# Kernel optimization log

Hardware: AMD Instinct MI355X
Metric: run time of the kernel (lower is better)

Reference implementation:

```python
import jax, jax.numpy as jnp
import numpy as np

N = 100000   # nodes
E = 1600000  # edges (avg degree 16)
D = 64       # in = hidden = out channels
NEG_SLOPE = 0.2
EPS_IN = 1e-5


def setup_inputs() -> dict:
    key = jax.random.key(0)
    ks = jax.random.split(key, 24)
    s = 0.05
    p = lambda k, shape: jax.random.normal(k, shape, jnp.float32) * s
    inp = {
        "x": jax.random.normal(ks[0], (N, D), jnp.float32),
        "edge_index": jax.random.randint(ks[1], (2, E), 0, N, dtype=jnp.int64),
        "edge_attr": jax.random.normal(ks[2], (E, D), jnp.float32),
        # GATv2Conv #1: lin_l, lin_r (bias=True), lin_edge (bias=False), att, out bias
        "Wl1": p(ks[3], (D, D)), "bl1": p(ks[4], (D,)),
        "Wr1": p(ks[5], (D, D)), "br1": p(ks[6], (D,)),
        "We1": p(ks[7], (D, D)), "att1": p(ks[8], (D,)), "bo1": p(ks[9], (D,)),
        # GATv2Conv #2
        "Wl2": p(ks[10], (D, D)), "bl2": p(ks[11], (D,)),
        "Wr2": p(ks[12], (D, D)), "br2": p(ks[13], (D,)),
        "We2": p(ks[14], (D, D)), "att2": p(ks[15], (D,)), "bo2": p(ks[16], (D,)),
        # skip linear
        "Wskip": p(ks[17], (D, D)), "bskip": p(ks[18], (D,)),
    }
    return inp


def _instance_norm(h):
    # InstanceNorm1d on a 2D [N, C] input -> per-row normalization over C, no affine
    mu = h.mean(-1, keepdims=True)
    var = ((h - mu) ** 2).mean(-1, keepdims=True)
    return (h - mu) * jax.lax.rsqrt(var + EPS_IN)


def _gatv2(x, src, dst, edge_attr, Wl, bl, Wr, br, We, att, bo):
    xl = x @ Wl.T + bl          # source-side transform [N, D]
    xr = x @ Wr.T + br          # target-side transform [N, D]
    e = edge_attr @ We.T        # edge transform [E, D]
    m = xl[src] + xr[dst] + e   # per-edge pre-activation [E, D]
    score = jnp.where(m > 0, m, NEG_SLOPE * m) @ att  # [E]
    # segment softmax over edges sharing the same target node
    smax = jax.ops.segment_max(score, dst, num_segments=N)
    smax = jnp.where(jnp.isfinite(smax), smax, 0.0)
    es = jnp.exp(score - smax[dst])
    denom = jax.ops.segment_sum(es, dst, num_segments=N)
    alpha = es / (denom[dst] + 1e-16)  # [E]
    out = jax.ops.segment_sum(alpha[:, None] * xl[src], dst, num_segments=N)
    return out + bo


def reference(x, edge_index, edge_attr,
              Wl1, bl1, Wr1, br1, We1, att1, bo1,
              Wl2, bl2, Wr2, br2, We2, att2, bo2,
              Wskip, bskip):
    src, dst = edge_index[0], edge_index[1]
    h = jax.nn.relu(_gatv2(x, src, dst, edge_attr, Wl1, bl1, Wr1, br1, We1, att1, bo1))
    h = _instance_norm(h)
    h2 = jax.nn.relu(_gatv2(h, src, dst, edge_attr, Wl2, bl2, Wr2, br2, We2, att2, bo2)
                     + x @ Wskip.T + bskip)
    return _instance_norm(h2)
```

## Files before the change

### kernel.cpp

```cpp
#include <hip/hip_runtime.h>

#define DCH 64
#define NEG 0.2f

typedef float fx4 __attribute__((ext_vector_type(4)));
typedef short short8 __attribute__((ext_vector_type(8)));

__device__ __forceinline__ unsigned short f2bf(float f) {
    unsigned int u = __builtin_bit_cast(unsigned int, f);
    u += 0x7fffu + ((u >> 16) & 1u);
    return (unsigned short)(u >> 16);
}

__device__ __forceinline__ short8 pack_bf16x8(fx4 a, fx4 b) {
    short8 r;
    r[0] = (short)f2bf(a[0]); r[1] = (short)f2bf(a[1]);
    r[2] = (short)f2bf(a[2]); r[3] = (short)f2bf(a[3]);
    r[4] = (short)f2bf(b[0]); r[5] = (short)f2bf(b[1]);
    r[6] = (short)f2bf(b[2]); r[7] = (short)f2bf(b[3]);
    return r;
}

__global__ void k_zero(int* __restrict__ p, int n) {
    int i = blockIdx.x * blockDim.x + threadIdx.x;
    if (i < n) p[i] = 0;
}

__global__ void k_count(const int* __restrict__ ei, int* __restrict__ deg, int E) {
    int e = blockIdx.x * blockDim.x + threadIdx.x;
    if (e < E) atomicAdd(&deg[ei[E + e]], 1);
}

__global__ void k_scan1(const int* __restrict__ deg, int* __restrict__ rowptr,
                        int* __restrict__ bsum, int n) {
    __shared__ int s[256];
    int t = threadIdx.x;
    int base = blockIdx.x * 1024 + t * 4;
    int v[4]; int sum = 0;
    #pragma unroll
    for (int j = 0; j < 4; j++) {
        int idx = base + j;
        v[j] = (idx < n) ? deg[idx] : 0;
        sum += v[j];
    }
    s[t] = sum;
    __syncthreads();
    for (int o = 1; o < 256; o <<= 1) {
        int add = (t >= o) ? s[t - o] : 0;
        __syncthreads();
        s[t] += add;
        __syncthreads();
    }
    int excl = s[t] - sum;
    if (t == 255) bsum[blockIdx.x] = s[255];
    int run = excl;
    #pragma unroll
    for (int j = 0; j < 4; j++) {
        int idx = base + j;
        if (idx < n) rowptr[idx] = run;
        run += v[j];
    }
}

__global__ void k_scan2(int* __restrict__ bsum, int nb) {
    int run = 0;
    for (int i = 0; i < nb; i++) { int t = bsum[i]; bsum[i] = run; run += t; }
}

__global__ void k_scan3(int* __restrict__ rowptr, const int* __restrict__ bsum,
                        int n, int E) {
    int i = blockIdx.x * blockDim.x + threadIdx.x;
    if (i < n) rowptr[i] += bsum[i >> 10];
    if (i == 0) rowptr[n] = E;
}

__global__ void k_fill(const int* __restrict__ ei, const int* __restrict__ rowptr,
                       int* __restrict__ cnt, int* __restrict__ csrc,
                       int* __restrict__ ceid, int E) {
    int e = blockIdx.x * blockDim.x + threadIdx.x;
    if (e < E) {
        int t = ei[E + e];
        int p = rowptr[t] + atomicAdd(&cnt[t], 1);
        csrc[p] = ei[e];
        ceid[p] = e;
    }
}

__global__ __launch_bounds__(256) void k_node_gemm(
    const float* __restrict__ X, int nrows,
    const float* __restrict__ W0, const float* __restrict__ b0, float* __restrict__ O0,
    const float* __restrict__ W1, const float* __restrict__ b1, float* __restrict__ O1,
    const float* __restrict__ W2, const float* __restrict__ b2, float* __restrict__ O2)
{
    int wid = (blockIdx.x * blockDim.x + threadIdx.x) >> 6;
    int lane = threadIdx.x & 63;
    int ntiles = (nrows + 63) >> 6;
    if (wid >= ntiles) return;
    int base = wid * 64;
    int l15 = lane & 15, q = lane >> 4;

    short8 afr[4][2];
    #pragma unroll
    for (int mt = 0; mt < 4; mt++) {
        int row = base + mt * 16 + l15;
        if (row >= nrows) row = nrows - 1;
        const float* xp = X + (size_t)row * DCH + q * 8;
        #pragma unroll
        for (int kt = 0; kt < 2; kt++) {
            fx4 v0 = *(const fx4*)(xp + kt * 32);
            fx4 v1 = *(const fx4*)(xp + kt * 32 + 4);
            afr[mt][kt] = pack_bf16x8(v0, v1);
        }
    }

    const float* Ws[3] = {W0, W1, W2};
    const float* bs[3] = {b0, b1, b2};
    float* Os[3] = {O0, O1, O2};
    int nmat = O2 ? 3 : (O1 ? 2 : 1);

    for (int m = 0; m < nmat; m++) {
        const float* W = Ws[m];
        short8 bfr[4][2];
        #pragma unroll
        for (int nt = 0; nt < 4; nt++) {
            const float* wp = W + (nt * 16 + l15) * DCH + q * 8;
            #pragma unroll
            for (int kt = 0; kt < 2; kt++) {
                fx4 v0 = *(const fx4*)(wp + kt * 32);
                fx4 v1 = *(const fx4*)(wp + kt * 32 + 4);
                bfr[nt][kt] = pack_bf16x8(v0, v1);
            }
        }
        fx4 acc[4][4] = {};
        #pragma unroll
        for (int kt = 0; kt < 2; kt++)
            #pragma unroll
            for (int mt = 0; mt < 4; mt++)
                #pragma unroll
                for (int nt = 0; nt < 4; nt++)
                    acc[mt][nt] = __builtin_amdgcn_mfma_f32_16x16x32_bf16(
                        afr[mt][kt], bfr[nt][kt], acc[mt][nt], 0, 0, 0);

        float bias[4];
        #pragma unroll
        for (int nt = 0; nt < 4; nt++) bias[nt] = bs[m][nt * 16 + l15];
        float* O = Os[m];
        #pragma unroll
        for (int mt = 0; mt < 4; mt++) {
            #pragma unroll
            for (int r = 0; r < 4; r++) {
                int row = base + mt * 16 + q * 4 + r;
                if (row < nrows) {
                    #pragma unroll
                    for (int nt = 0; nt < 4; nt++)
                        O[(size_t)row * DCH + nt * 16 + l15] = acc[mt][nt][r] + bias[nt];
                }
            }
        }
    }
}

__global__ __launch_bounds__(256) void k_edge_score(
    const float* __restrict__ EA, const int* __restrict__ ei,
    const float* __restrict__ We, const float* __restrict__ att,
    const float* __restrict__ xl, const float* __restrict__ xr,
    float* __restrict__ es, int E)
{
    int wid = (blockIdx.x * blockDim.x + threadIdx.x) >> 6;
    int lane = threadIdx.x & 63;
    int l15 = lane & 15, q = lane >> 4;
    int base = wid * 64;
    if (base >= E) return;

    int s_me = ei[base + lane];
    int t_me = ei[E + base + lane];

    short8 bfr[4][2];
    #pragma unroll
    for (int nt = 0; nt < 4; nt++) {
        const float* wp = We + (nt * 16 + l15) * DCH + q * 8;
        #pragma unroll
        for (int kt = 0; kt < 2; kt++) {
            fx4 v0 = *(const fx4*)(wp + kt * 32);
            fx4 v1 = *(const fx4*)(wp + kt * 32 + 4);
            bfr[nt][kt] = pack_bf16x8(v0, v1);
        }
    }
    short8 afr[4][2];
    #pragma unroll
    for (int mt = 0; mt < 4; mt++) {
        const float* p = EA + (size_t)(base + mt * 16 + l15) * DCH + q * 8;
        #pragma unroll
        for (int kt = 0; kt < 2; kt++) {
            fx4 v0 = *(const fx4*)(p + kt * 32);
            fx4 v1 = *(const fx4*)(p + kt * 32 + 4);
            afr[mt][kt] = pack_bf16x8(v0, v1);
        }
    }
    fx4 acc[4][4] = {};
    #pragma unroll
    for (int kt = 0; kt < 2; kt++)
        #pragma unroll
        for (int mt = 0; mt < 4; mt++)
            #pragma unroll
            for (int nt = 0; nt < 4; nt++)
                acc[mt][nt] = __builtin_amdgcn_mfma_f32_16x16x32_bf16(
                    afr[mt][kt], bfr[nt][kt], acc[mt][nt], 0, 0, 0);

    float attr[4];
    #pragma unroll
    for (int nt = 0; nt < 4; nt++) attr[nt] = att[nt * 16 + l15];

    #pragma unroll
    for (int mt = 0; mt < 4; mt++) {
        #pragma unroll
        for (int r = 0; r < 4; r++) {
            int m = mt * 16 + q * 4 + r;
            int sm = __shfl(s_me, m);
            int tm = __shfl(t_me, m);
            const float* xls = xl + (size_t)sm * DCH + l15;
            const float* xrt = xr + (size_t)tm * DCH + l15;
            float p = 0.f;
            #pragma unroll
            for (int nt = 0; nt < 4; nt++) {
                float z = acc[mt][nt][r] + xls[nt * 16] + xrt[nt * 16];
                float lr = fmaxf(z, 0.f) + NEG * fminf(z, 0.f);
                p = fmaf(attr[nt], lr, p);
            }
            p += __shfl_xor(p, 1);
            p += __shfl_xor(p, 2);
            p += __shfl_xor(p, 4);
            p += __shfl_xor(p, 8);
            if (l15 == mt * 4 + r) es[base + m] = __expf(p);
        }
    }
}

__global__ __launch_bounds__(256) void k_pull(
    const int* __restrict__ rowptr, const int* __restrict__ csrc,
    const int* __restrict__ ceid, const float* __restrict__ es,
    const float* __restrict__ xl, const float* __restrict__ bo,
    const float* __restrict__ skip, float* __restrict__ out, int n_nodes)
{
    int wid = (blockIdx.x * blockDim.x + threadIdx.x) >> 6;
    int lane = threadIdx.x & 63;
    if (wid >= n_nodes) return;
    int r0 = rowptr[wid], r1 = rowptr[wid + 1];
    float acc = 0.f, den = 0.f;
    for (int b = r0; b < r1; b += 64) {
        int cnt = min(64, r1 - b);
        int sj = 0; float wj = 0.f;
        if (lane < cnt) {
            sj = csrc[b + lane];
            wj = es[ceid[b + lane]];
        }
        for (int i = 0; i < cnt; i++) {
            int s = __shfl(sj, i);
            float w = __shfl(wj, i);
            acc = fmaf(w, xl[(size_t)s * DCH + lane], acc);
            den += w;
        }
    }
    float v = acc / (den + 1e-16f) + bo[lane];
    if (skip) v += skip[(size_t)wid * DCH + lane];
    v = fmaxf(v, 0.f);
    float mu = v;
    #pragma unroll
    for (int o = 1; o < 64; o <<= 1) mu += __shfl_xor(mu, o);
    mu *= (1.f / 64.f);
    float d = v - mu;
    float var = d * d;
    #pragma unroll
    for (int o = 1; o < 64; o <<= 1) var += __shfl_xor(var, o);
    var *= (1.f / 64.f);
    out[(size_t)wid * DCH + lane] = d * rsqrtf(var + 1e-5f);
}

extern "C" void kernel_launch(void* const* d_in, const int* in_sizes, int n_in,
                              void* d_out, int out_size, void* d_ws, size_t ws_size,
                              hipStream_t stream) {
    const float* x    = (const float*)d_in[0];
    const int*   ei   = (const int*)d_in[1];
    const float* ea   = (const float*)d_in[2];
    const float* Wl1  = (const float*)d_in[3];
    const float* bl1  = (const float*)d_in[4];
    const float* Wr1  = (const float*)d_in[5];
    const float* br1  = (const float*)d_in[6];
    const float* We1  = (const float*)d_in[7];
    const float* att1 = (const float*)d_in[8];
    const float* bo1  = (const float*)d_in[9];
    const float* Wl2  = (const float*)d_in[10];
    const float* bl2  = (const float*)d_in[11];
    const float* Wr2  = (const float*)d_in[12];
    const float* br2  = (const float*)d_in[13];
    const float* We2  = (const float*)d_in[14];
    const float* att2 = (const float*)d_in[15];
    const float* bo2  = (const float*)d_in[16];
    const float* Wsk  = (const float*)d_in[17];
    const float* bsk  = (const float*)d_in[18];
    float* out = (float*)d_out;

    const int N = in_sizes[0] / DCH;
    const int E = in_sizes[1] / 2;

    char* ws = (char*)d_ws;
    size_t off = 0;
    float* xl   = (float*)(ws + off); off += (size_t)N * DCH * 4;
    float* xr   = (float*)(ws + off); off += (size_t)N * DCH * 4;
    float* h    = (float*)(ws + off); off += (size_t)N * DCH * 4;
    float* S    = (float*)(ws + off); off += (size_t)N * DCH * 4;
    float* es   = (float*)(ws + off); off += (size_t)E * 4;
    int* rowptr = (int*)(ws + off);   off += (size_t)(N + 1) * 4;
    int* degcnt = (int*)(ws + off);   off += (size_t)(2 * N) * 4;
    int* csrc   = (int*)(ws + off);   off += (size_t)E * 4;
    int* ceid   = (int*)(ws + off);   off += (size_t)E * 4;
    int* bsum   = (int*)(ws + off);   off += 256 * 4;
    int* deg = degcnt;
    int* cnt = degcnt + N;

    const int nb = (N + 1023) / 1024;

    k_zero<<<(2 * N + 255) / 256, 256, 0, stream>>>(degcnt, 2 * N);
    k_count<<<(E + 255) / 256, 256, 0, stream>>>(ei, deg, E);
    k_scan1<<<nb, 256, 0, stream>>>(deg, rowptr, bsum, N);
    k_scan2<<<1, 1, 0, stream>>>(bsum, nb);
    k_scan3<<<(N + 255) / 256, 256, 0, stream>>>(rowptr, bsum, N, E);
    k_fill<<<(E + 255) / 256, 256, 0, stream>>>(ei, rowptr, cnt, csrc, ceid, E);

    const int node_tiles = (N + 63) / 64;
    const int ng_blocks = (node_tiles + 3) / 4;
    const int eg_blocks = (E + 255) / 256;
    const int pull_blocks = (N + 3) / 4;

    k_node_gemm<<<ng_blocks, 256, 0, stream>>>(x, N,
        Wl1, bl1, xl, Wr1, br1, xr, Wsk, bsk, S);
    k_edge_score<<<eg_blocks, 256, 0, stream>>>(ea, ei, We1, att1, xl, xr, es, E);
    k_pull<<<pull_blocks, 256, 0, stream>>>(rowptr, csrc, ceid, es, xl, bo1,
                                            nullptr, h, N);
    k_node_gemm<<<ng_blocks, 256, 0, stream>>>(h, N,
        Wl2, bl2, xl, Wr2, br2, xr, nullptr, nullptr, nullptr);
    k_edge_score<<<eg_blocks, 256, 0, stream>>>(ea, ei, We2, att2, xl, xr, es, E);
    k_pull<<<pull_blocks, 256, 0, stream>>>(rowptr, csrc, ceid, es, xl, bo2,
                                            S, out, N);
}
```

Measured before the change: 1.386 ms.

## Fuse edge scoring into CSR pull and precompute both edge transforms in bf16

Both layers' edge-attribute transforms now run in one kernel that reads edge_attr once and writes the results as bf16 in CSR (destination-sorted) order via an inverse permutation. The attention score, exp and weighted aggregation move into the per-node pull kernel, with xl stored in bf16 and the next neighbour prefetched, which removes the separate per-edge score kernels and their scattered gathers. The cost is a large bf16 edge buffer per layer, scattered row writes in the transform kernel, and a 64-lane shuffle reduction per edge inside the pull loop. It also drops the max subtraction from the softmax, as the previous code already did.

```diff
diff --git a/kernel.cpp b/kernel.cpp
--- a/kernel.cpp
+++ b/kernel.cpp
@@ -10,6 +10,10 @@
     unsigned int u = __builtin_bit_cast(unsigned int, f);
     u += 0x7fffu + ((u >> 16) & 1u);
     return (unsigned short)(u >> 16);
+}
+__device__ __forceinline__ float bf2f(unsigned short h) {
+    unsigned int u = ((unsigned int)h) << 16;
+    return __builtin_bit_cast(float, u);
 }
 
 __device__ __forceinline__ short8 pack_bf16x8(fx4 a, fx4 b) {
@@ -76,21 +80,21 @@
 
 __global__ void k_fill(const int* __restrict__ ei, const int* __restrict__ rowptr,
                        int* __restrict__ cnt, int* __restrict__ csrc,
-                       int* __restrict__ ceid, int E) {
+                       int* __restrict__ iperm, int E) {
     int e = blockIdx.x * blockDim.x + threadIdx.x;
     if (e < E) {
         int t = ei[E + e];
         int p = rowptr[t] + atomicAdd(&cnt[t], 1);
         csrc[p] = ei[e];
-        ceid[p] = e;
+        iperm[e] = p;
     }
 }
 
 __global__ __launch_bounds__(256) void k_node_gemm(
     const float* __restrict__ X, int nrows,
-    const float* __restrict__ W0, const float* __restrict__ b0, float* __restrict__ O0,
-    const float* __restrict__ W1, const float* __restrict__ b1, float* __restrict__ O1,
-    const float* __restrict__ W2, const float* __restrict__ b2, float* __restrict__ O2)
+    const float* __restrict__ Wl, const float* __restrict__ bl, unsigned short* __restrict__ XLB,
+    const float* __restrict__ Wr, const float* __restrict__ br, float* __restrict__ XR,
+    const float* __restrict__ Wsk, const float* __restrict__ bsk, float* __restrict__ S)
 {
     int wid = (blockIdx.x * blockDim.x + threadIdx.x) >> 6;
     int lane = threadIdx.x & 63;
@@ -113,10 +117,9 @@
         }
     }
 
-    const float* Ws[3] = {W0, W1, W2};
-    const float* bs[3] = {b0, b1, b2};
-    float* Os[3] = {O0, O1, O2};
-    int nmat = O2 ? 3 : (O1 ? 2 : 1);
+    const float* Ws[3] = {Wl, Wr, Wsk};
+    const float* bs[3] = {bl, br, bsk};
+    int nmat = S ? 3 : 2;
 
     for (int m = 0; m < nmat; m++) {
         const float* W = Ws[m];
@@ -144,7 +147,6 @@
         float bias[4];
         #pragma unroll
         for (int nt = 0; nt < 4; nt++) bias[nt] = bs[m][nt * 16 + l15];
-        float* O = Os[m];
         #pragma unroll
         for (int mt = 0; mt < 4; mt++) {
             #pragma unroll
@@ -152,19 +154,25 @@
                 int row = base + mt * 16 + q * 4 + r;
                 if (row < nrows) {
                     #pragma unroll
-                    for (int nt = 0; nt < 4; nt++)
-                        O[(size_t)row * DCH + nt * 16 + l15] = acc[mt][nt][r] + bias[nt];
+                    for (int nt = 0; nt < 4; nt++) {
+                        float v = acc[mt][nt][r] + bias[nt];
+                        if (m == 0)
+                            XLB[(size_t)row * DCH + nt * 16 + l15] = f2bf(v);
+                        else if (m == 1)
+                            XR[(size_t)row * DCH + nt * 16 + l15] = v;
+                        else
+                            S[(size_t)row * DCH + nt * 16 + l15] = v;
+                    }
                 }
             }
         }
     }
 }
 
-__global__ __launch_bounds__(256) void k_edge_score(
-    const float* __restrict__ EA, const int* __restrict__ ei,
-    const float* __restrict__ We, const float* __restrict__ att,
-    const float* __restrict__ xl, const float* __restrict__ xr,
-    float* __restrict__ es, int E)
+__global__ __launch_bounds__(256) void k_edge_tf(
+    const float* __restrict__ EA, const int* __restrict__ iperm,
+    const float* __restrict__ We1, const float* __restrict__ We2,
+    unsigned short* __restrict__ E1, unsigned short* __restrict__ E2, int E)
 {
     int wid = (blockIdx.x * blockDim.x + threadIdx.x) >> 6;
     int lane = threadIdx.x & 63;
@@ -172,24 +180,13 @@
     int base = wid * 64;
     if (base >= E) return;
 
-    int s_me = ei[base + lane];
-    int t_me = ei[E + base + lane];
-
-    short8 bfr[4][2];
-    #pragma unroll
-    for (int nt = 0; nt < 4; nt++) {
-        const float* wp = We + (nt * 16 + l15) * DCH + q * 8;
-        #pragma unroll
-        for (int kt = 0; kt < 2; kt++) {
-            fx4 v0 = *(const fx4*)(wp + kt * 32);
-            fx4 v1 = *(const fx4*)(wp + kt * 32 + 4);
-            bfr[nt][kt] = pack_bf16x8(v0, v1);
-        }
-    }
+    int p_me = iperm[min(base + lane, E - 1)];
+
     short8 afr[4][2];
     #pragma unroll
     for (int mt = 0; mt < 4; mt++) {
-        const float* p = EA + (size_t)(base + mt * 16 + l15) * DCH + q * 8;
+        int row = min(base + mt * 16 + l15, E - 1);
+        const float* p = EA + (size_t)row * DCH + q * 8;
         #pragma unroll
         for (int kt = 0; kt < 2; kt++) {
             fx4 v0 = *(const fx4*)(p + kt * 32);
@@ -197,70 +194,95 @@
             afr[mt][kt] = pack_bf16x8(v0, v1);
         }
     }
-    fx4 acc[4][4] = {};
-    #pragma unroll
-    for (int kt = 0; kt < 2; kt++)
-        #pragma unroll
-        for (int mt = 0; mt < 4; mt++)
-            #pragma unroll
-            for (int nt = 0; nt < 4; nt++)
-                acc[mt][nt] = __builtin_amdgcn_mfma_f32_16x16x32_bf16(
-                    afr[mt][kt], bfr[nt][kt], acc[mt][nt], 0, 0, 0);
-
-    float attr[4];
-    #pragma unroll
-    for (int nt = 0; nt < 4; nt++) attr[nt] = att[nt * 16 + l15];
-
-    #pragma unroll
-    for (int mt = 0; mt < 4; mt++) {
-        #pragma unroll
-        for (int r = 0; r < 4; r++) {
-            int m = mt * 16 + q * 4 + r;
-            int sm = __shfl(s_me, m);
-            int tm = __shfl(t_me, m);
-            const float* xls = xl + (size_t)sm * DCH + l15;
-            const float* xrt = xr + (size_t)tm * DCH + l15;
-            float p = 0.f;
-            #pragma unroll
-            for (int nt = 0; nt < 4; nt++) {
-                float z = acc[mt][nt][r] + xls[nt * 16] + xrt[nt * 16];
-                float lr = fmaxf(z, 0.f) + NEG * fminf(z, 0.f);
-                p = fmaf(attr[nt], lr, p);
-            }
-            p += __shfl_xor(p, 1);
-            p += __shfl_xor(p, 2);
-            p += __shfl_xor(p, 4);
-            p += __shfl_xor(p, 8);
-            if (l15 == mt * 4 + r) es[base + m] = __expf(p);
+
+    const float* Ws[2] = {We1, We2};
+    unsigned short* Es[2] = {E1, E2};
+    #pragma unroll
+    for (int lyr = 0; lyr < 2; lyr++) {
+        const float* W = Ws[lyr];
+        short8 bfr[4][2];
+        #pragma unroll
+        for (int nt = 0; nt < 4; nt++) {
+            const float* wp = W + (nt * 16 + l15) * DCH + q * 8;
+            #pragma unroll
+            for (int kt = 0; kt < 2; kt++) {
+                fx4 v0 = *(const fx4*)(wp + kt * 32);
+                fx4 v1 = *(const fx4*)(wp + kt * 32 + 4);
+                bfr[nt][kt] = pack_bf16x8(v0, v1);
+            }
+        }
+        fx4 acc[4][4] = {};
+        #pragma unroll
+        for (int kt = 0; kt < 2; kt++)
+            #pragma unroll
+            for (int mt = 0; mt < 4; mt++)
+                #pragma unroll
+                for (int nt = 0; nt < 4; nt++)
+                    acc[mt][nt] = __builtin_amdgcn_mfma_f32_16x16x32_bf16(
+                        afr[mt][kt], bfr[nt][kt], acc[mt][nt], 0, 0, 0);
+
+        unsigned short* Eo = Es[lyr];
+        #pragma unroll
+        for (int mt = 0; mt < 4; mt++) {
+            #pragma unroll
+            for (int r = 0; r < 4; r++) {
+                int m = mt * 16 + q * 4 + r;
+                int pm = __shfl(p_me, m);
+                if (base + m < E) {
+                    #pragma unroll
+                    for (int nt = 0; nt < 4; nt++)
+                        Eo[(size_t)pm * DCH + nt * 16 + l15] = f2bf(acc[mt][nt][r]);
+                }
+            }
         }
     }
 }
 
 __global__ __launch_bounds__(256) void k_pull(
     const int* __restrict__ rowptr, const int* __restrict__ csrc,
-    const int* __restrict__ ceid, const float* __restrict__ es,
-    const float* __restrict__ xl, const float* __restrict__ bo,
-    const float* __restrict__ skip, float* __restrict__ out, int n_nodes)
+    const unsigned short* __restrict__ ECSR, const unsigned short* __restrict__ XLB,
+    const float* __restrict__ XR, const float* __restrict__ att,
+    const float* __restrict__ bo, const float* __restrict__ skip,
+    float* __restrict__ out, int n_nodes)
 {
     int wid = (blockIdx.x * blockDim.x + threadIdx.x) >> 6;
     int lane = threadIdx.x & 63;
     if (wid >= n_nodes) return;
     int r0 = rowptr[wid], r1 = rowptr[wid + 1];
+    float xr_l = XR[(size_t)wid * DCH + lane];
+    float att_l = att[lane];
     float acc = 0.f, den = 0.f;
+
     for (int b = r0; b < r1; b += 64) {
         int cnt = min(64, r1 - b);
-        int sj = 0; float wj = 0.f;
-        if (lane < cnt) {
-            sj = csrc[b + lane];
-            wj = es[ceid[b + lane]];
-        }
+        int sj = 0;
+        if (lane < cnt) sj = csrc[b + lane];
+        int s0 = __shfl(sj, 0);
+        unsigned short xl_pf = XLB[(size_t)s0 * DCH + lane];
+        unsigned short e_pf = ECSR[(size_t)b * DCH + lane];
         for (int i = 0; i < cnt; i++) {
-            int s = __shfl(sj, i);
-            float w = __shfl(wj, i);
-            acc = fmaf(w, xl[(size_t)s * DCH + lane], acc);
+            float xlv = bf2f(xl_pf);
+            float ev = bf2f(e_pf);
+            if (i + 1 < cnt) {
+                int s1 = __shfl(sj, i + 1);
+                xl_pf = XLB[(size_t)s1 * DCH + lane];
+                e_pf = ECSR[(size_t)(b + i + 1) * DCH + lane];
+            }
+            float z = xlv + xr_l + ev;
+            float lr = fmaxf(z, 0.f) + NEG * fminf(z, 0.f);
+            float t = att_l * lr;
+            t += __shfl_xor(t, 1);
+            t += __shfl_xor(t, 2);
+            t += __shfl_xor(t, 4);
+            t += __shfl_xor(t, 8);
+            t += __shfl_xor(t, 16);
+            t += __shfl_xor(t, 32);
+            float w = __expf(t);
+            acc = fmaf(w, xlv, acc);
             den += w;
         }
     }
+
     float v = acc / (den + 1e-16f) + bo[lane];
     if (skip) v += skip[(size_t)wid * DCH + lane];
     v = fmaxf(v, 0.f);
@@ -305,15 +327,16 @@
 
     char* ws = (char*)d_ws;
     size_t off = 0;
-    float* xl   = (float*)(ws + off); off += (size_t)N * DCH * 4;
+    unsigned short* e1  = (unsigned short*)(ws + off); off += (size_t)E * DCH * 2;
+    unsigned short* e2  = (unsigned short*)(ws + off); off += (size_t)E * DCH * 2;
+    unsigned short* xlb = (unsigned short*)(ws + off); off += (size_t)N * DCH * 2;
     float* xr   = (float*)(ws + off); off += (size_t)N * DCH * 4;
     float* h    = (float*)(ws + off); off += (size_t)N * DCH * 4;
     float* S    = (float*)(ws + off); off += (size_t)N * DCH * 4;
-    float* es   = (float*)(ws + off); off += (size_t)E * 4;
     int* rowptr = (int*)(ws + off);   off += (size_t)(N + 1) * 4;
     int* degcnt = (int*)(ws + off);   off += (size_t)(2 * N) * 4;
     int* csrc   = (int*)(ws + off);   off += (size_t)E * 4;
-    int* ceid   = (int*)(ws + off);   off += (size_t)E * 4;
+    int* iperm  = (int*)(ws + off);   off += (size_t)E * 4;
     int* bsum   = (int*)(ws + off);   off += 256 * 4;
     int* deg = degcnt;
     int* cnt = degcnt + N;
@@ -325,21 +348,21 @@
     k_scan1<<<nb, 256, 0, stream>>>(deg, rowptr, bsum, N);
     k_scan2<<<1, 1, 0, stream>>>(bsum, nb);
     k_scan3<<<(N + 255) / 256, 256, 0, stream>>>(rowptr, bsum, N, E);
-    k_fill<<<(E + 255) / 256, 256, 0, stream>>>(ei, rowptr, cnt, csrc, ceid, E);
+    k_fill<<<(E + 255) / 256, 256, 0, stream>>>(ei, rowptr, cnt, csrc, iperm, E);
 
     const int node_tiles = (N + 63) / 64;
     const int ng_blocks = (node_tiles + 3) / 4;
-    const int eg_blocks = (E + 255) / 256;
+    const int eg_blocks = (E / 64 + 3) / 4;
     const int pull_blocks = (N + 3) / 4;
 
-    k_node_gemm<<<ng_blocks, 256, 0, stream>>>(x, N,
-        Wl1, bl1, xl, Wr1, br1, xr, Wsk, bsk, S);
-    k_edge_score<<<eg_blocks, 256, 0, stream>>>(ea, ei, We1, att1, xl, xr, es, E);
-    k_pull<<<pull_blocks, 256, 0, stream>>>(rowptr, csrc, ceid, es, xl, bo1,
+    k_edge_tf<<<eg_blocks, 256, 0, stream>>>(ea, iperm, We1, We2, e1, e2, E);
+
+    k_node_gemm<<<ng_blocks, 256, 0, stream>>>(x, N, Wl1, bl1, xlb, Wr1, br1, xr,
+                                               Wsk, bsk, S);
+    k_pull<<<pull_blocks, 256, 0, stream>>>(rowptr, csrc, e1, xlb, xr, att1, bo1,
                                             nullptr, h, N);
-    k_node_gemm<<<ng_blocks, 256, 0, stream>>>(h, N,
-        Wl2, bl2, xl, Wr2, br2, xr, nullptr, nullptr, nullptr);
-    k_edge_score<<<eg_blocks, 256, 0, stream>>>(ea, ei, We2, att2, xl, xr, es, E);
-    k_pull<<<pull_blocks, 256, 0, stream>>>(rowptr, csrc, ceid, es, xl, bo2,
+    k_node_gemm<<<ng_blocks, 256, 0, stream>>>(h, N, Wl2, bl2, xlb, Wr2, br2, xr,
+                                               nullptr, nullptr, nullptr);
+    k_pull<<<pull_blocks, 256, 0, stream>>>(rowptr, csrc, e2, xlb, xr, att2, bo2,
                                             S, out, N);
 }
```

After: 1.299 ms. 1.07x faster.
